# Optimization experiments

Measured on AMD Instinct MI355X. Metric: run time of the kernel, lower is better.

Reference implementation:

```python
import jax, jax.numpy as jnp
import numpy as np

SEQ_LEN = 8192
D_MODEL = 1024
D_K = 128
D_V = 128


def setup_inputs() -> dict:
    key = jax.random.key(0)
    kx, kq, kk, kv = jax.random.split(key, 4)
    # xavier-uniform scale for (out, in) linear weights
    def xavier(k, out_f, in_f):
        lim = np.sqrt(6.0 / (in_f + out_f))
        return jax.random.uniform(k, (out_f, in_f), jnp.float32, -lim, lim)
    return {
        "X": jax.random.normal(kx, (SEQ_LEN, D_MODEL), jnp.float32),
        "Wq": xavier(kq, D_K, D_MODEL),
        "Wk": xavier(kk, D_K, D_MODEL),
        "Wv": xavier(kv, D_V, D_MODEL),
    }


def reference(X, Wq, Wk, Wv):
    # X: (S, d_model); W*: (d_k, d_model) torch Linear weights (y = x @ W.T)
    S = X.shape[0]
    Q = X @ Wq.T                      # (S, d_k)
    K = X @ Wk.T                      # (S, d_k)
    V = X @ Wv.T                      # (S, d_v)
    scale = jnp.sqrt(jnp.asarray(D_K, X.dtype))
    scores = (Q @ K.T) / scale        # (S, S)
    causal = jnp.tril(jnp.ones((S, S), bool))
    scores = jnp.where(causal, scores, -jnp.inf)
    weights = jax.nn.softmax(scores, axis=1)
    # dropout p=0.0 -> identity
    Z = weights @ V                   # (S, d_v)
    return Z
```

## Files before the change

kernel.cpp:

```cpp
#include <hip/hip_runtime.h>
#include <hip/hip_bf16.h>

#define S_LEN 8192
#define DM    1024
#define DK    128
#define KSTR  136
#define VSTR  72
#define SLOTD 2112
#define NCMAX 16

typedef __attribute__((ext_vector_type(8))) short bf16x8;
typedef __attribute__((ext_vector_type(8))) _Float16 f16x8;
typedef __attribute__((ext_vector_type(4))) float f32x4;
typedef __attribute__((ext_vector_type(16))) float f32x16;

__device__ __forceinline__ f32x4 mfma16f(f16x8 a, f16x8 b, f32x4 c) {
    return __builtin_amdgcn_mfma_f32_16x16x32_f16(a, b, c, 0, 0, 0);
}
__device__ __forceinline__ f32x16 mfma32(bf16x8 a, bf16x8 b, f32x16 c) {
    return __builtin_amdgcn_mfma_f32_32x32x16_bf16(a, b, c, 0, 0, 0);
}

__device__ __forceinline__ ushort f2bf(float f) {
    unsigned u = __builtin_bit_cast(unsigned, f);
    u += 0x7FFFu + ((u >> 16) & 1u);
    return (ushort)(u >> 16);
}

__device__ __forceinline__ ushort f2h(float f) {
    return __builtin_bit_cast(ushort, (_Float16)f);
}

__device__ __forceinline__ uint cvt_pk_bf16(float a, float b) {
    uint r;
    asm("v_cvt_pk_bf16_f32 %0, %1, %2" : "=v"(r) : "v"(a), "v"(b));
    return r;
}

__global__ __launch_bounds__(256, 1)
void convert_w_kernel(const float* __restrict__ Wq,
                      const float* __restrict__ Wk,
                      const float* __restrict__ Wv,
                      _Float16* __restrict__ Wh) {
    const int NW4 = DK * DM / 4;
    const int i = blockIdx.x * 256 + threadIdx.x;
    const int which = i / NW4;
    const int off = i - which * NW4;
    const float4 v = ((const float4*)(which == 0 ? Wq : (which == 1 ? Wk : Wv)))[off];
    union { _Float16 h[4]; uint2 u; } p;
    p.h[0] = (_Float16)v.x; p.h[1] = (_Float16)v.y;
    p.h[2] = (_Float16)v.z; p.h[3] = (_Float16)v.w;
    *(uint2*)(Wh + (size_t)which * (DK * DM) + (size_t)off * 4) = p.u;
}

__global__ __launch_bounds__(256)
void proj_gemm_kernel(const float* __restrict__ X,
                      const _Float16* __restrict__ Wh,
                      ushort* __restrict__ Qb,
                      ushort* __restrict__ Kb,
                      ushort* __restrict__ Vtb) {
    __shared__ _Float16 Ash[2][16 * 32];
    __shared__ _Float16 Bsh[2][384 * 32];

    const int tid  = threadIdx.x;
    const int lane = tid & 63;
    const int quad = lane >> 4;
    const int l15  = lane & 15;
    const int wv   = tid >> 6;
    const int m0   = blockIdx.x * 16;
    const int arow = tid >> 3, ac4 = tid & 7;

    f32x4 acc[3][2];
#pragma unroll
    for (int nb = 0; nb < 3; ++nb)
#pragma unroll
        for (int ni = 0; ni < 2; ++ni) acc[nb][ni] = (f32x4){0.f, 0.f, 0.f, 0.f};

#define STAGE_B(KK, BUF)                                                       \
    {                                                                          \
        _Pragma("unroll")                                                      \
        for (int s_ = tid; s_ < 1536; s_ += 256) {                             \
            const int row_ = s_ >> 2, sg_ = s_ & 3;                            \
            __builtin_amdgcn_global_load_lds(                                  \
                (const __attribute__((address_space(1))) void*)(Wh + (size_t)row_ * DM + (KK) + sg_ * 8), \
                (__attribute__((address_space(3))) void*)(Bsh[BUF] + s_ * 8), 16, 0, 0); \
        }                                                                      \
    }
#define LOAD_A(DST, KK)                                                        \
    if (tid < 128) (DST) = *(const float4*)(X + (size_t)(m0 + arow) * DM + (KK) + ac4 * 4);
#define WRITE_A(SRC, BUF)                                                      \
    if (tid < 128) {                                                           \
        union { _Float16 h[4]; uint2 u; } pa_;                                 \
        pa_.h[0] = (_Float16)(SRC).x; pa_.h[1] = (_Float16)(SRC).y;            \
        pa_.h[2] = (_Float16)(SRC).z; pa_.h[3] = (_Float16)(SRC).w;            \
        *(uint2*)(Ash[BUF] + arow * 32 + ac4 * 4) = pa_.u;                     \
    }
#define COMPUTE(BUF)                                                           \
    {                                                                          \
        const f16x8 af_ = *(const f16x8*)(Ash[BUF] + l15 * 32 + quad * 8);     \
        _Pragma("unroll")                                                      \
        for (int nb_ = 0; nb_ < 3; ++nb_)                                      \
            _Pragma("unroll")                                                  \
            for (int ni_ = 0; ni_ < 2; ++ni_) {                                \
                const f16x8 bf_ = *(const f16x8*)(Bsh[BUF] + (nb_ * 128 + wv * 32 + ni_ * 16 + l15) * 32 + quad * 8); \
                acc[nb_][ni_] = mfma16f(af_, bf_, acc[nb_][ni_]);              \
            }                                                                  \
    }

    float4 ra, rb;
    LOAD_A(ra, 0)
    LOAD_A(rb, 32)
    STAGE_B(0, 0)
    WRITE_A(ra, 0)
    __syncthreads();

    for (int kk = 0; kk < DM; kk += 64) {
        if (kk + 32 < DM) STAGE_B(kk + 32, 1)
        if (kk + 64 < DM) LOAD_A(ra, kk + 64)
        COMPUTE(0)
        if (kk + 32 < DM) WRITE_A(rb, 1)
        __syncthreads();
        if (kk + 32 < DM) {
            if (kk + 64 < DM) STAGE_B(kk + 64, 0)
            if (kk + 96 < DM) LOAD_A(rb, kk + 96)
            COMPUTE(1)
            if (kk + 64 < DM) WRITE_A(ra, 0)
            __syncthreads();
        }
    }
#undef STAGE_B
#undef LOAD_A
#undef WRITE_A
#undef COMPUTE

    const float scq = 0.088388347648318447f * 1.4426950408889634f;
#pragma unroll
    for (int ni = 0; ni < 2; ++ni) {
        const int n = wv * 32 + ni * 16 + l15;
#pragma unroll
        for (int r = 0; r < 4; ++r)
            Qb[(size_t)(m0 + quad * 4 + r) * DK + n] = f2bf(acc[0][ni][r] * scq);
#pragma unroll
        for (int r = 0; r < 4; ++r)
            Kb[(size_t)(m0 + quad * 4 + r) * DK + n] = f2bf(acc[1][ni][r]);
        union { ushort h[4]; uint2 u; } p;
#pragma unroll
        for (int r = 0; r < 4; ++r) p.h[r] = f2bf(acc[2][ni][r]);
        *(uint2*)(Vtb + (size_t)n * S_LEN + m0 + quad * 4) = p.u;
    }
}

__global__ __launch_bounds__(256, 2)
void flash_partial_kernel(const ushort* __restrict__ Qg,
                          const ushort* __restrict__ Kg,
                          const ushort* __restrict__ Vtg,
                          float* __restrict__ Part) {
    __shared__ __align__(16) ushort Ks [2][64 * KSTR];
    __shared__ __align__(16) ushort Vts[2][128 * VSTR];

    int rem = 543 - (int)blockIdx.x;
    int qb = 0;
    for (;;) {
        const int nc = (2 * qb + 9) >> 3;
        if (rem < nc) break;
        rem -= nc; ++qb;
    }
    const int NC    = (2 * qb + 9) >> 3;
    const int chunk = rem;
    const int nkt   = 2 * qb + 2;
    const int kt_lo = chunk * nkt / NC;
    const int kt_hi = (chunk + 1) * nkt / NC;

    const int tid  = threadIdx.x;
    const int wv   = tid >> 6;
    const int lane = tid & 63;
    const int l31  = lane & 31;
    const int hi   = lane >> 5;
    const int q0w  = qb * 128 + wv * 32;
    const int qrow = q0w + l31;

    bf16x8 qf[8];
    {
        const ushort* qp = Qg + (size_t)qrow * DK + hi * 8;
#pragma unroll
        for (int i = 0; i < 8; ++i) qf[i] = *(const bf16x8*)(qp + i * 16);
    }

    float m_ = -__builtin_inff();
    float l_ = 0.f;
    f32x16 acc[4];
#pragma unroll
    for (int dt = 0; dt < 4; ++dt)
#pragma unroll
        for (int j = 0; j < 16; ++j) acc[dt][j] = 0.f;

    bf16x8 stg[8];
#define LOAD_TILE(K0)                                                          \
    {                                                                          \
        const int k0_ = (K0);                                                  \
        _Pragma("unroll")                                                      \
        for (int i = 0; i < 8; ++i) {                                          \
            const int c = tid + (i << 8);                                      \
            if (c < 1024) {                                                    \
                const int row = c >> 4, ch = c & 15;                           \
                stg[i] = *(const bf16x8*)(Kg + (size_t)(k0_ + row) * DK + ch * 8); \
            } else {                                                           \
                const int cc = c - 1024;                                       \
                const int row = cc >> 3, ch = cc & 7;                          \
                stg[i] = *(const bf16x8*)(Vtg + (size_t)row * S_LEN + k0_ + ch * 8); \
            }                                                                  \
        }                                                                      \
    }
#define WRITE_BUF(B)                                                           \
    {                                                                          \
        ushort* Kb_ = Ks[B]; ushort* Vb_ = Vts[B];                             \
        _Pragma("unroll")                                                      \
        for (int i = 0; i < 8; ++i) {                                          \
            const int c = tid + (i << 8);                                      \
            if (c < 1024) {                                                    \
                const int row = c >> 4, ch = c & 15;                           \
                *(bf16x8*)(Kb_ + row * KSTR + ch * 8) = stg[i];                \
            } else {                                                           \
                const int cc = c - 1024;                                       \
                const int row = cc >> 3, ch = cc & 7;                          \
                const int s_lo = ((ch & 1) << 2) + (((ch >> 1) & 1) << 4) + ((ch >> 2) << 5); \
                union { bf16x8 v; uint2 q2[2]; } u;                            \
                u.v = stg[i];                                                  \
                ushort* vb = Vb_ + row * VSTR + s_lo;                          \
                *(uint2*)vb       = u.q2[0];                                   \
                *(uint2*)(vb + 8) = u.q2[1];                                   \
            }                                                                  \
        }                                                                      \
    }

    LOAD_TILE(kt_lo * 64)
    WRITE_BUF(0)
    if (kt_lo + 1 < kt_hi) LOAD_TILE((kt_lo + 1) * 64)
    __syncthreads();

    for (int kt = kt_lo; kt < kt_hi; ++kt) {
        const int k0 = kt * 64;
        const int cb = (kt - kt_lo) & 1;
        const ushort* ks = Ks[cb];
        const ushort* vs = Vts[cb];
        const bool prc = (k0 <= q0w);

        f32x16 Sr0, Sr1;
        if (prc) {
            __builtin_amdgcn_s_setprio(1);
#pragma unroll
            for (int j = 0; j < 16; ++j) { Sr0[j] = 0.f; Sr1[j] = 0.f; }
            const ushort* ka0 = ks + l31 * KSTR + hi * 8;
            const ushort* ka1 = ka0 + 32 * KSTR;
#pragma unroll
            for (int i = 0; i < 8; ++i)
                Sr0 = mfma32(*(const bf16x8*)(ka0 + i * 16), qf[i], Sr0);
#pragma unroll
            for (int i = 0; i < 8; ++i)
                Sr1 = mfma32(*(const bf16x8*)(ka1 + i * 16), qf[i], Sr1);
            __builtin_amdgcn_s_setprio(0);
        }

        if (kt + 1 < kt_hi) {
            WRITE_BUF(cb ^ 1)
            if (kt + 2 < kt_hi) LOAD_TILE((kt + 2) * 64)
        }

        if (prc) {
            if (k0 + 63 > q0w) {
#pragma unroll
                for (int r = 0; r < 16; ++r) {
                    const int krow = (r & 3) + 8 * (r >> 2) + 4 * hi;
                    if (k0 + krow > qrow)      Sr0[r] = -__builtin_inff();
                    if (k0 + 32 + krow > qrow) Sr1[r] = -__builtin_inff();
                }
            }

            float pmax = Sr0[0];
#pragma unroll
            for (int r = 1; r < 16; ++r) pmax = fmaxf(pmax, Sr0[r]);
#pragma unroll
            for (int r = 0; r < 16; ++r) pmax = fmaxf(pmax, Sr1[r]);
            pmax = fmaxf(pmax, __shfl_xor(pmax, 32));
            if (__any(pmax > m_ + 8.f)) {
                const float mnew = fmaxf(m_, pmax);
                const float al = __builtin_amdgcn_exp2f(m_ - mnew);
                m_ = mnew;
                l_ *= al;
#pragma unroll
                for (int dt = 0; dt < 4; ++dt)
#pragma unroll
                    for (int j = 0; j < 16; ++j) acc[dt][j] *= al;
            }
            float rs = 0.f;
            uint pfa[16];
            {
                float p0[16], p1[16];
#pragma unroll
                for (int r = 0; r < 16; ++r) { p0[r] = __builtin_amdgcn_exp2f(Sr0[r] - m_); rs += p0[r]; }
#pragma unroll
                for (int r = 0; r < 16; ++r) { p1[r] = __builtin_amdgcn_exp2f(Sr1[r] - m_); rs += p1[r]; }
#pragma unroll
                for (int j = 0; j < 4; ++j) {
                    pfa[j]      = cvt_pk_bf16(p0[2 * j],     p0[2 * j + 1]);
                    pfa[4 + j]  = cvt_pk_bf16(p0[8 + 2 * j], p0[8 + 2 * j + 1]);
                    pfa[8 + j]  = cvt_pk_bf16(p1[2 * j],     p1[2 * j + 1]);
                    pfa[12 + j] = cvt_pk_bf16(p1[8 + 2 * j], p1[8 + 2 * j + 1]);
                }
            }
            rs += __shfl_xor(rs, 32);
            l_ += rs;

            __builtin_amdgcn_s_setprio(1);
#pragma unroll
            for (int kc = 0; kc < 4; ++kc) {
                union { uint u[4]; bf16x8 v; } pu;
#pragma unroll
                for (int j = 0; j < 4; ++j) pu.u[j] = pfa[4 * kc + j];
                const ushort* va = vs + l31 * VSTR + kc * 16 + hi * 8;
#pragma unroll
                for (int dt = 0; dt < 4; ++dt)
                    acc[dt] = mfma32(*(const bf16x8*)(va + dt * 32 * VSTR), pu.v, acc[dt]);
            }
            __builtin_amdgcn_s_setprio(0);
        }
        __syncthreads();
    }
#undef LOAD_TILE
#undef WRITE_BUF

    const int qt32 = qb * 4 + wv;
    float* slot = Part + (size_t)(qt32 * NCMAX + chunk) * SLOTD;
    if (hi == 0) {
        slot[l31]      = m_;
        slot[32 + l31] = l_;
    }
    uint* slotO = (uint*)(slot + 64);
#pragma unroll
    for (int dt = 0; dt < 4; ++dt)
#pragma unroll
        for (int s = 0; s < 4; ++s) {
            uint2 w;
            w.x = (uint)f2h(acc[dt][4 * s])     | ((uint)f2h(acc[dt][4 * s + 1]) << 16);
            w.y = (uint)f2h(acc[dt][4 * s + 2]) | ((uint)f2h(acc[dt][4 * s + 3]) << 16);
            *(uint2*)(slotO + l31 * 64 + dt * 16 + s * 4 + hi * 2) = w;
        }
}

__global__ __launch_bounds__(256)
void flash_merge_kernel(const float* __restrict__ Part, float* __restrict__ Out) {
    __shared__ float Ms[32], Ls[32];
    __shared__ float Sc[16][32];
    const int qt   = blockIdx.x >> 1;
    const int half = blockIdx.x & 1;
    const int qb = qt >> 2;
    const int P  = (2 * qb + 9) >> 3;
    const int q0 = qt * 32;
    const int tid = threadIdx.x;
    const float* base = Part + (size_t)qt * NCMAX * SLOTD;

    if (tid < 32) {
        float M = -__builtin_inff();
        for (int p = 0; p < P; ++p) M = fmaxf(M, base[p * SLOTD + tid]);
        float L = 0.f;
        for (int p = 0; p < P; ++p)
            L += base[p * SLOTD + 32 + tid] * exp2f(base[p * SLOTD + tid] - M);
        Ms[tid] = M; Ls[tid] = L;
    }
    __syncthreads();
    for (int j = tid; j < 512; j += 256) {
        const int p = j >> 5, row = j & 31;
        Sc[p][row] = (p < P) ? exp2f(base[p * SLOTD + row] - Ms[row]) : 0.f;
    }
    __syncthreads();

#pragma unroll
    for (int j = tid; j < 1024; j += 256) {
        const int row = j >> 5, c2 = (j & 31) + half * 32;
        float o0 = 0.f, o1 = 0.f;
        for (int p = 0; p < P; ++p) {
            const uint u = ((const uint*)(base + p * SLOTD + 64))[row * 64 + c2];
            const float sc = Sc[p][row];
            o0 += (float)__builtin_bit_cast(_Float16, (ushort)(u & 0xFFFF)) * sc;
            o1 += (float)__builtin_bit_cast(_Float16, (ushort)(u >> 16)) * sc;
        }
        const float inv = 1.0f / Ls[row];
        float2 o; o.x = o0 * inv; o.y = o1 * inv;
        *(float2*)(Out + (size_t)(q0 + row) * DK + c2 * 2) = o;
    }
}

extern "C" void kernel_launch(void* const* d_in, const int* in_sizes, int n_in,
                              void* d_out, int out_size, void* d_ws, size_t ws_size,
                              hipStream_t stream) {
    const float* X  = (const float*)d_in[0];
    const float* Wq = (const float*)d_in[1];
    const float* Wk = (const float*)d_in[2];
    const float* Wv = (const float*)d_in[3];
    ushort* ws  = (ushort*)d_ws;
    ushort* Qb  = ws;
    ushort* Kb  = ws + (size_t)S_LEN * DK;
    ushort* Vtb = ws + 2 * (size_t)S_LEN * DK;
    _Float16* Wh = (_Float16*)(ws + 3 * (size_t)S_LEN * DK);
    float* Part = (float*)(Wh + (size_t)3 * DK * DM);
    float* Out = (float*)d_out;

    convert_w_kernel<<<384, 256, 0, stream>>>(Wq, Wk, Wv, Wh);
    proj_gemm_kernel<<<512, 256, 0, stream>>>(X, Wh, Qb, Kb, Vtb);
    flash_partial_kernel<<<544, 256, 0, stream>>>(Qb, Kb, Vtb, Part);
    flash_merge_kernel<<<512, 256, 0, stream>>>(Part, Out);
}
```

Baseline: 169.4 us.

## Fuse split-K merge into flash partial kernel via atomic last-block counter

Removes the separate merge kernel launch. Each wave atomically increments a per-query-tile counter after writing its partial slot, and the last-arriving wave performs the log-sum-exp merge and writes the output. Counters are zeroed in the weight-convert kernel. This saves a launch and a grid-wide dependency, at the cost of serialized merge work in a single wave per tile and extra fences and atomics.

```diff
diff --git a/kernel.cpp b/kernel.cpp
--- a/kernel.cpp
+++ b/kernel.cpp
@@ -41,7 +41,9 @@
 void convert_w_kernel(const float* __restrict__ Wq,
                       const float* __restrict__ Wk,
                       const float* __restrict__ Wv,
-                      _Float16* __restrict__ Wh) {
+                      _Float16* __restrict__ Wh,
+                      unsigned* __restrict__ cnt) {
+    if (blockIdx.x == 0) cnt[threadIdx.x] = 0u;
     const int NW4 = DK * DM / 4;
     const int i = blockIdx.x * 256 + threadIdx.x;
     const int which = i / NW4;
@@ -154,7 +156,9 @@
 void flash_partial_kernel(const ushort* __restrict__ Qg,
                           const ushort* __restrict__ Kg,
                           const ushort* __restrict__ Vtg,
-                          float* __restrict__ Part) {
+                          float* __restrict__ Part,
+                          unsigned* __restrict__ cnt,
+                          float* __restrict__ Out) {
     __shared__ __align__(16) ushort Ks [2][64 * KSTR];
     __shared__ __align__(16) ushort Vts[2][128 * VSTR];
 
@@ -345,48 +349,43 @@
             w.y = (uint)f2h(acc[dt][4 * s + 2]) | ((uint)f2h(acc[dt][4 * s + 3]) << 16);
             *(uint2*)(slotO + l31 * 64 + dt * 16 + s * 4 + hi * 2) = w;
         }
-}
-
-__global__ __launch_bounds__(256)
-void flash_merge_kernel(const float* __restrict__ Part, float* __restrict__ Out) {
-    __shared__ float Ms[32], Ls[32];
-    __shared__ float Sc[16][32];
-    const int qt   = blockIdx.x >> 1;
-    const int half = blockIdx.x & 1;
-    const int qb = qt >> 2;
-    const int P  = (2 * qb + 9) >> 3;
-    const int q0 = qt * 32;
-    const int tid = threadIdx.x;
-    const float* base = Part + (size_t)qt * NCMAX * SLOTD;
-
-    if (tid < 32) {
+
+    __threadfence();
+    unsigned old = 0;
+    if (lane == 0) old = atomicAdd(cnt + qt32, 1u);
+    old = __shfl(old, 0);
+    if (old == (unsigned)(NC - 1)) {
+        __threadfence();
+        const float* base = Part + (size_t)qt32 * NCMAX * SLOTD;
         float M = -__builtin_inff();
-        for (int p = 0; p < P; ++p) M = fmaxf(M, base[p * SLOTD + tid]);
+        for (int p = 0; p < NC; ++p) M = fmaxf(M, base[p * SLOTD + l31]);
         float L = 0.f;
-        for (int p = 0; p < P; ++p)
-            L += base[p * SLOTD + 32 + tid] * exp2f(base[p * SLOTD + tid] - M);
-        Ms[tid] = M; Ls[tid] = L;
-    }
-    __syncthreads();
-    for (int j = tid; j < 512; j += 256) {
-        const int p = j >> 5, row = j & 31;
-        Sc[p][row] = (p < P) ? exp2f(base[p * SLOTD + row] - Ms[row]) : 0.f;
-    }
-    __syncthreads();
-
-#pragma unroll
-    for (int j = tid; j < 1024; j += 256) {
-        const int row = j >> 5, c2 = (j & 31) + half * 32;
-        float o0 = 0.f, o1 = 0.f;
-        for (int p = 0; p < P; ++p) {
-            const uint u = ((const uint*)(base + p * SLOTD + 64))[row * 64 + c2];
-            const float sc = Sc[p][row];
-            o0 += (float)__builtin_bit_cast(_Float16, (ushort)(u & 0xFFFF)) * sc;
-            o1 += (float)__builtin_bit_cast(_Float16, (ushort)(u >> 16)) * sc;
-        }
-        const float inv = 1.0f / Ls[row];
-        float2 o; o.x = o0 * inv; o.y = o1 * inv;
-        *(float2*)(Out + (size_t)(q0 + row) * DK + c2 * 2) = o;
+        for (int p = 0; p < NC; ++p)
+            L += base[p * SLOTD + 32 + l31] * __builtin_amdgcn_exp2f(base[p * SLOTD + l31] - M);
+        const float inv = 1.0f / L;
+        const int q0 = qt32 * 32;
+#pragma unroll
+        for (int g = 0; g < 4; ++g) {
+            float o[16];
+#pragma unroll
+            for (int j = 0; j < 16; ++j) o[j] = 0.f;
+            for (int p = 0; p < NC; ++p) {
+                const float sc = __builtin_amdgcn_exp2f(base[p * SLOTD + l31] - M);
+                const uint* so = (const uint*)(base + p * SLOTD + 64) + l31 * 64 + hi * 32 + g * 8;
+#pragma unroll
+                for (int j = 0; j < 8; ++j) {
+                    const uint u = so[j];
+                    o[2 * j]     += (float)__builtin_bit_cast(_Float16, (ushort)(u & 0xFFFF)) * sc;
+                    o[2 * j + 1] += (float)__builtin_bit_cast(_Float16, (ushort)(u >> 16)) * sc;
+                }
+            }
+            float2* op = (float2*)(Out + (size_t)(q0 + l31) * DK) + hi * 32 + g * 8;
+#pragma unroll
+            for (int j = 0; j < 8; ++j) {
+                float2 t; t.x = o[2 * j] * inv; t.y = o[2 * j + 1] * inv;
+                op[j] = t;
+            }
+        }
     }
 }
 
@@ -403,10 +402,10 @@
     ushort* Vtb = ws + 2 * (size_t)S_LEN * DK;
     _Float16* Wh = (_Float16*)(ws + 3 * (size_t)S_LEN * DK);
     float* Part = (float*)(Wh + (size_t)3 * DK * DM);
+    unsigned* cnt = (unsigned*)(Part + (size_t)256 * NCMAX * SLOTD);
     float* Out = (float*)d_out;
 
-    convert_w_kernel<<<384, 256, 0, stream>>>(Wq, Wk, Wv, Wh);
+    convert_w_kernel<<<384, 256, 0, stream>>>(Wq, Wk, Wv, Wh, cnt);
     proj_gemm_kernel<<<512, 256, 0, stream>>>(X, Wh, Qb, Kb, Vtb);
-    flash_partial_kernel<<<544, 256, 0, stream>>>(Qb, Kb, Vtb, Part);
-    flash_merge_kernel<<<512, 256, 0, stream>>>(Part, Out);
-}
+    flash_partial_kernel<<<544, 256, 0, stream>>>(Qb, Kb, Vtb, Part, cnt, Out);
+}
```

After: 275.8 us. 1.63x slower.
